# Optimization experiments

Measured on AMD Instinct MI355X. Metric: run time of the kernel, lower is better.

## Reference

```python
import jax, jax.numpy as jnp
import numpy as np

P = 2        # patch_size
HEADS = 1


def _conv(x, w, b, groups=1):
    # NCHW conv, kernel 3x3, SAME padding (stride 1)
    y = jax.lax.conv_general_dilated(
        x, w, window_strides=(1, 1), padding='SAME',
        dimension_numbers=('NCHW', 'OIHW', 'NCHW'),
        feature_group_count=groups)
    return y + b[None, :, None, None]


def _unfold(x, p):
    # torch.nn.Unfold(kernel=p, stride=p): [B,C,h,w] -> [B, C*p*p, n]
    B, C, h, w = x.shape
    x = x.reshape(B, C, h // p, p, w // p, p)
    x = x.transpose(0, 1, 3, 5, 2, 4)  # (B, C, ph, pw, h/p, w/p)
    return x.reshape(B, C * p * p, (h // p) * (w // p))


def _fold(x, p, h, w):
    # inverse of _unfold (non-overlapping patches)
    B = x.shape[0]
    C = x.shape[1] // (p * p)
    x = x.reshape(B, C, p, p, h // p, w // p)
    x = x.transpose(0, 1, 4, 2, 5, 3)  # (B, C, h/p, ph, w/p, pw)
    return x.reshape(B, C, h, w)


def setup_inputs() -> dict:
    key = jax.random.key(0)
    ks = jax.random.split(key, 9)
    c = 64
    x = jax.random.normal(ks[0], (2, 5, c, 64, 64), jnp.float32)
    wq = jax.random.normal(ks[1], (c, 1, 3, 3), jnp.float32) * 0.1
    bq = jax.random.normal(ks[2], (c,), jnp.float32) * 0.1
    wk = jax.random.normal(ks[3], (c, 1, 3, 3), jnp.float32) * 0.1
    bk = jax.random.normal(ks[4], (c,), jnp.float32) * 0.1
    wv = jax.random.normal(ks[5], (c, c, 3, 3), jnp.float32) * 0.05
    bv = jax.random.normal(ks[6], (c,), jnp.float32) * 0.1
    wc = jax.random.normal(ks[7], (c, c, 3, 3), jnp.float32) * 0.05
    bc = jax.random.normal(ks[8], (c,), jnp.float32) * 0.1
    return {"x": x, "wq": wq, "bq": bq, "wk": wk, "bk": bk,
            "wv": wv, "bv": bv, "wc": wc, "bc": bc}


def reference(x, wq, bq, wk, bk, wv, bv, wc, bc):
    b, t, c, h, w = x.shape
    p, H = P, HEADS
    D = p * p * c           # 256
    d = D // H              # per-head dim
    n = (h // p) * (w // p)  # tokens per frame

    xf = x.reshape(b * t, c, h, w)
    q = _conv(xf, wq, bq, groups=c)   # depthwise
    k = _conv(xf, wk, bk, groups=c)   # depthwise
    v = _conv(xf, wv, bv)             # dense conv

    def to_tokens(y):
        # [bt, D, n] -> [b, H, d, t*n]
        u = _unfold(y, p).reshape(b, t, H, d, n)
        return u.transpose(0, 2, 3, 1, 4).reshape(b, H, d, t * n)

    uq, uk, uv = to_tokens(q), to_tokens(k), to_tokens(v)

    attn = jnp.einsum('bhdi,bhdj->bhij', uq, uk) * (d ** -0.5)
    attn = jax.nn.softmax(attn, axis=-1)           # [b,H,tn,tn]
    ax = jnp.einsum('bhij,bhdj->bhid', attn, uv)   # [b,H,tn,d]

    ax = ax.reshape(b, H, t, n, d).transpose(0, 2, 1, 4, 3).reshape(b * t, D, n)
    feat = _fold(ax, p, h, w)                      # [bt, c, h, w]
    out = _conv(feat, wc, bc).reshape(x.shape) + x
    return out
```

## Files before the change

### kernel.cpp

```cpp
#include <hip/hip_runtime.h>
#include <hip/hip_bf16.h>

typedef __attribute__((ext_vector_type(8))) short short8;
typedef __attribute__((ext_vector_type(8))) unsigned short ushort8;
typedef __attribute__((ext_vector_type(4))) unsigned short ushort4v;
typedef __attribute__((ext_vector_type(4))) float f32x4;

#define NTOK 5120
#define DDIM 256
#define NJC 8

__device__ __forceinline__ unsigned short f2bf(float f) {
  union { float f; unsigned int u; } x; x.f = f;
  unsigned int r = x.u + 0x7FFFu + ((x.u >> 16) & 1u);
  return (unsigned short)(r >> 16);
}
__device__ __forceinline__ float bf2f(unsigned short u) {
  union { unsigned int i; float f; } x; x.i = ((unsigned int)u) << 16; return x.f;
}

__global__ __launch_bounds__(256) void qk_gen(
    const float* __restrict__ xin, const float* __restrict__ wq,
    const float* __restrict__ bq, const float* __restrict__ wk,
    const float* __restrict__ bk, unsigned short* __restrict__ qt,
    unsigned short* __restrict__ kt)
{
  const int ch = blockIdx.x;
  const int bt = blockIdx.y;
  const int b = bt / 5, tf = bt % 5;
  const int tid = threadIdx.x;
  const float* xp = xin + ((size_t)bt * 64 + ch) * 4096;
  float wqv[9], wkv[9];
  #pragma unroll
  for (int i = 0; i < 9; i++) { wqv[i] = wq[ch * 9 + i]; wkv[i] = wk[ch * 9 + i]; }
  const float bqv = bq[ch], bkv = bk[ch];

  #pragma unroll
  for (int p = 0; p < 4; p++) {
    int pid = tid + p * 256;
    int gy = pid >> 5, gx = pid & 31;
    float v[4][4];
    #pragma unroll
    for (int r = 0; r < 4; r++) {
      int yy = 2 * gy - 1 + r;
      #pragma unroll
      for (int cc = 0; cc < 4; cc++) {
        int xx = 2 * gx - 1 + cc;
        bool ok = (yy >= 0) && (yy < 64) && (xx >= 0) && (xx < 64);
        v[r][cc] = ok ? xp[yy * 64 + xx] : 0.f;
      }
    }
    unsigned short qo[4], ko[4];
    #pragma unroll
    for (int py = 0; py < 2; py++)
      #pragma unroll
      for (int px = 0; px < 2; px++) {
        float aq = bqv, ak = bkv;
        #pragma unroll
        for (int dy = 0; dy < 3; dy++)
          #pragma unroll
          for (int dx = 0; dx < 3; dx++) {
            float xv = v[py + dy][px + dx];
            aq += wqv[dy * 3 + dx] * xv;
            ak += wkv[dy * 3 + dx] * xv;
          }
        qo[py * 2 + px] = f2bf(aq);
        ko[py * 2 + px] = f2bf(ak);
      }
    size_t base = ((size_t)(b * NTOK + tf * 1024 + pid)) * DDIM + ch * 4;
    ushort4v qv = { qo[0], qo[1], qo[2], qo[3] };
    ushort4v kv = { ko[0], ko[1], ko[2], ko[3] };
    *(ushort4v*)(qt + base) = qv;
    *(ushort4v*)(kt + base) = kv;
  }
}

__global__ __launch_bounds__(256) void wt_gen(
    const float* __restrict__ w0, const float* __restrict__ w1,
    unsigned short* __restrict__ o0, unsigned short* __restrict__ o1)
{
  const int tap = blockIdx.x;
  const float* src = blockIdx.y ? w1 : w0;
  unsigned short* dst = blockIdx.y ? o1 : o0;
  const int t = threadIdx.x;
  #pragma unroll
  for (int i = 0; i < 16; i++) {
    int oi = t + i * 256;
    dst[tap * 4096 + oi] = f2bf(src[(size_t)oi * 9 + tap]);
  }
}

template<int MODE>
__global__ __launch_bounds__(256) void conv_mfma(
    const float* __restrict__ src, const unsigned short* __restrict__ wt,
    const float* __restrict__ bias, const float* __restrict__ resid,
    float* __restrict__ dstf, unsigned short* __restrict__ vt)
{
  const int strip = blockIdx.x;
  const int bt = blockIdx.y;
  const int y0 = strip * 2;
  const int tid = threadIdx.x;
  const int sw = tid >> 6, lane = tid & 63;
  const int ry = sw >> 1, ch = sw & 1;
  const int g = lane >> 4, c = lane & 15;

  __shared__ __align__(16) unsigned short lds_in[4 * 66 * 64];
  __shared__ __align__(16) unsigned short lds_w[64 * 64];

  {
    const int rr = lane >> 4;
    const int cb = lane & 15;
    const int row = y0 - 1 + rr;
    const bool rok = (row >= 0) && (row < 64);
    #pragma unroll
    for (int pp = 0; pp < 8; ++pp) {
      const int ci0 = sw * 16 + pp * 2;
      f32x4 va = { 0.f, 0.f, 0.f, 0.f }, vb = { 0.f, 0.f, 0.f, 0.f };
      if (rok) {
        va = *(const f32x4*)(src + ((size_t)(bt * 64 + ci0)) * 4096 + row * 64 + cb * 4);
        vb = *(const f32x4*)(src + ((size_t)(bt * 64 + ci0 + 1)) * 4096 + row * 64 + cb * 4);
      }
      char* rbase = (char*)lds_in + (rr * 66) * 128 + (ci0 & 7) * 2;
      const int sl = ci0 >> 3;
      #pragma unroll
      for (int q = 0; q < 4; ++q) {
        int lcol = cb * 4 + q + 1;
        unsigned int pk = (unsigned int)f2bf(va[q]) | ((unsigned int)f2bf(vb[q]) << 16);
        *(unsigned int*)(rbase + lcol * 128 + ((sl ^ (lcol & 7)) * 16)) = pk;
      }
      if (cb == 0)  *(unsigned int*)(rbase + ((sl ^ 0) * 16)) = 0u;
      if (cb == 15) *(unsigned int*)(rbase + 65 * 128 + ((sl ^ 1) * 16)) = 0u;
    }
  }

  f32x4 acc[2][4];
  #pragma unroll
  for (int ct = 0; ct < 2; ct++)
    #pragma unroll
    for (int xt = 0; xt < 4; xt++) acc[ct][xt] = (f32x4){ 0.f, 0.f, 0.f, 0.f };

  #pragma unroll 1
  for (int tap = 0; tap < 9; ++tap) {
    __syncthreads();
    {
      const unsigned short* wp = wt + tap * 4096;
      #pragma unroll
      for (int h = 0; h < 2; ++h) {
        int el = h * 2048 + tid * 8;
        int co = el >> 6, sl = (el & 63) >> 3;
        short8 wv8 = *(const short8*)(wp + el);
        *(short8*)((char*)lds_w + co * 128 + ((sl ^ (co & 7)) * 16)) = wv8;
      }
    }
    __syncthreads();
    const int dy = tap / 3 - 1, dx = tap % 3 - 1;
    const int rowp = ry + 1 + dy;
    #pragma unroll
    for (int kblk = 0; kblk < 2; ++kblk) {
      short8 af[2], bf[4];
      #pragma unroll
      for (int ct = 0; ct < 2; ++ct) {
        int co = ch * 32 + ct * 16 + c;
        af[ct] = *(const short8*)((char*)lds_w + co * 128 + (((kblk * 4 + g) ^ (co & 7)) * 16));
      }
      #pragma unroll
      for (int xt = 0; xt < 4; ++xt) {
        int lcol = xt * 16 + c + dx + 1;
        bf[xt] = *(const short8*)((char*)lds_in + (rowp * 66 + lcol) * 128 + (((kblk * 4 + g) ^ (lcol & 7)) * 16));
      }
      #pragma unroll
      for (int ct = 0; ct < 2; ++ct)
        #pragma unroll
        for (int xt = 0; xt < 4; ++xt)
          acc[ct][xt] = __builtin_amdgcn_mfma_f32_16x16x32_bf16(af[ct], bf[xt], acc[ct][xt], 0, 0, 0);
    }
  }

  const int y = y0 + ry;
  if (MODE == 0) {
    const int b = bt / 5, tf = bt % 5;
    const int py = y & 1, gy = y >> 1;
    #pragma unroll
    for (int ct = 0; ct < 2; ++ct)
      #pragma unroll
      for (int r = 0; r < 4; ++r) {
        const int co = ch * 32 + ct * 16 + g * 4 + r;
        const float bv = bias[co];
        #pragma unroll
        for (int xt = 0; xt < 4; ++xt) {
          int x = xt * 16 + c;
          int d = co * 4 + py * 2 + (x & 1);
          int tok = tf * 1024 + gy * 32 + (x >> 1);
          vt[((size_t)(b * DDIM + d)) * NTOK + tok] = f2bf(acc[ct][xt][r] + bv);
        }
      }
  } else {
    #pragma unroll
    for (int ct = 0; ct < 2; ++ct)
      #pragma unroll
      for (int r = 0; r < 4; ++r) {
        const int co = ch * 32 + ct * 16 + g * 4 + r;
        const float bv = bias[co];
        const size_t rowb = ((size_t)(bt * 64 + co)) * 4096 + (size_t)y * 64;
        #pragma unroll
        for (int xt = 0; xt < 4; ++xt) {
          int x = xt * 16 + c;
          dstf[rowb + x] = acc[ct][xt][r] + bv + resid[rowb + x];
        }
      }
  }
}

__global__ __launch_bounds__(256) void attn_kernel(
    const unsigned short* __restrict__ qt, const unsigned short* __restrict__ kt,
    const unsigned short* __restrict__ vt, float* __restrict__ po,
    float* __restrict__ pm, float* __restrict__ pl)
{
  const int wgid = blockIdx.x;
  const int chunk = wgid / 320;
  const int within = wgid % 320;
  const int slice = chunk * 8 + (within & 7);
  const int b = slice >> 3;
  const int jc = slice & 7;
  const int i0 = (within >> 3) * 128;
  const int jchunk = NTOK / NJC;
  const int tid = threadIdx.x;
  const int w = tid >> 6, lane = tid & 63;
  const int g = lane >> 4, c = lane & 15;

  __shared__ __align__(16) unsigned short lds_k[64 * 256];
  __shared__ __align__(16) unsigned short lds_v[256 * 64];
  __shared__ __align__(16) unsigned short lds_p[4 * 16 * 64];

  short8 qf[2][8];
  #pragma unroll
  for (int st = 0; st < 2; st++) {
    const unsigned short* qr = qt + ((size_t)(b * NTOK + i0 + w * 32 + st * 16 + c)) * DDIM + g * 8;
    #pragma unroll
    for (int kb = 0; kb < 8; kb++) qf[st][kb] = *(const short8*)(qr + kb * 32);
  }
  f32x4 o[32];
  #pragma unroll
  for (int i = 0; i < 32; i++) o[i] = (f32x4){ 0.f, 0.f, 0.f, 0.f };
  float m[2][4], l[2][4];
  #pragma unroll
  for (int st = 0; st < 2; st++)
    #pragma unroll
    for (int r = 0; r < 4; r++) { m[st][r] = -1e30f; l[st][r] = 0.f; }

  const int sr = tid >> 5, sc = tid & 31;
  const int vdr = tid >> 3, vcc = tid & 7;
  char* pb = (char*)lds_p + w * 2048;

  const int jbeg = jc * jchunk;
  for (int j0 = jbeg; j0 < jbeg + jchunk; j0 += 64) {
    #pragma unroll
    for (int p = 0; p < 8; p++) {
      int row = sr + p * 8;
      short8 kv = *(const short8*)(kt + ((size_t)(b * NTOK + j0 + row)) * DDIM + sc * 8);
      *(short8*)((char*)lds_k + row * 512 + ((sc ^ (row & 7)) * 16)) = kv;
    }
    #pragma unroll
    for (int p = 0; p < 8; p++) {
      int dd = vdr + p * 32;
      short8 vv = *(const short8*)(vt + ((size_t)(b * DDIM + dd)) * NTOK + j0 + vcc * 8);
      *(short8*)((char*)lds_v + dd * 128 + ((vcc ^ (dd & 7)) * 16)) = vv;
    }
    __syncthreads();

    f32x4 s0[4], s1[4];
    #pragma unroll
    for (int js = 0; js < 4; js++) {
      s0[js] = (f32x4){ 0.f, 0.f, 0.f, 0.f };
      s1[js] = (f32x4){ 0.f, 0.f, 0.f, 0.f };
      int row = js * 16 + c;
      int sw2 = row & 7;
      #pragma unroll
      for (int kb = 0; kb < 8; kb++) {
        short8 kf = *(const short8*)((char*)lds_k + row * 512 + (((kb * 4 + g) ^ sw2) * 16));
        s0[js] = __builtin_amdgcn_mfma_f32_16x16x32_bf16(qf[0][kb], kf, s0[js], 0, 0, 0);
        s1[js] = __builtin_amdgcn_mfma_f32_16x16x32_bf16(qf[1][kb], kf, s1[js], 0, 0, 0);
      }
    }
    short8 pf[2][2];
    {
      float pvv[4][4], alpha[4];
      #pragma unroll
      for (int r = 0; r < 4; r++) {
        float mx = fmaxf(fmaxf(s0[0][r], s0[1][r]), fmaxf(s0[2][r], s0[3][r])) * 0.0625f;
        #pragma unroll
        for (int off = 1; off < 16; off <<= 1) mx = fmaxf(mx, __shfl_xor(mx, off));
        float mn = fmaxf(m[0][r], mx);
        alpha[r] = __expf(m[0][r] - mn);
        float p0 = __expf(s0[0][r] * 0.0625f - mn);
        float p1 = __expf(s0[1][r] * 0.0625f - mn);
        float p2 = __expf(s0[2][r] * 0.0625f - mn);
        float p3 = __expf(s0[3][r] * 0.0625f - mn);
        pvv[0][r] = p0; pvv[1][r] = p1; pvv[2][r] = p2; pvv[3][r] = p3;
        float sum = p0 + p1 + p2 + p3;
        #pragma unroll
        for (int off = 1; off < 16; off <<= 1) sum += __shfl_xor(sum, off);
        l[0][r] = l[0][r] * alpha[r] + sum;
        m[0][r] = mn;
      }
      f32x4 av = { alpha[0], alpha[1], alpha[2], alpha[3] };
      #pragma unroll
      for (int ds = 0; ds < 16; ds++) o[ds] *= av;
      #pragma unroll
      for (int js = 0; js < 4; js++)
        #pragma unroll
        for (int r = 0; r < 4; r++) {
          int row = 4 * g + r;
          int slot = (js * 2 + (c >> 3)) ^ (row & 7);
          *(unsigned short*)(pb + row * 128 + slot * 16 + (c & 7) * 2) = f2bf(pvv[js][r]);
        }
      #pragma unroll
      for (int k2 = 0; k2 < 2; k2++)
        pf[0][k2] = *(short8*)(pb + c * 128 + (((k2 * 4 + g) ^ (c & 7)) * 16));
    }
    {
      float pvv[4][4], alpha[4];
      #pragma unroll
      for (int r = 0; r < 4; r++) {
        float mx = fmaxf(fmaxf(s1[0][r], s1[1][r]), fmaxf(s1[2][r], s1[3][r])) * 0.0625f;
        #pragma unroll
        for (int off = 1; off < 16; off <<= 1) mx = fmaxf(mx, __shfl_xor(mx, off));
        float mn = fmaxf(m[1][r], mx);
        alpha[r] = __expf(m[1][r] - mn);
        float p0 = __expf(s1[0][r] * 0.0625f - mn);
        float p1 = __expf(s1[1][r] * 0.0625f - mn);
        float p2 = __expf(s1[2][r] * 0.0625f - mn);
        float p3 = __expf(s1[3][r] * 0.0625f - mn);
        pvv[0][r] = p0; pvv[1][r] = p1; pvv[2][r] = p2; pvv[3][r] = p3;
        float sum = p0 + p1 + p2 + p3;
        #pragma unroll
        for (int off = 1; off < 16; off <<= 1) sum += __shfl_xor(sum, off);
        l[1][r] = l[1][r] * alpha[r] + sum;
        m[1][r] = mn;
      }
      f32x4 av = { alpha[0], alpha[1], alpha[2], alpha[3] };
      #pragma unroll
      for (int ds = 0; ds < 16; ds++) o[16 + ds] *= av;
      #pragma unroll
      for (int js = 0; js < 4; js++)
        #pragma unroll
        for (int r = 0; r < 4; r++) {
          int row = 4 * g + r;
          int slot = (js * 2 + (c >> 3)) ^ (row & 7);
          *(unsigned short*)(pb + row * 128 + slot * 16 + (c & 7) * 2) = f2bf(pvv[js][r]);
        }
      #pragma unroll
      for (int k2 = 0; k2 < 2; k2++)
        pf[1][k2] = *(short8*)(pb + c * 128 + (((k2 * 4 + g) ^ (c & 7)) * 16));
    }
    #pragma unroll
    for (int ds = 0; ds < 16; ds++) {
      int vrow = ds * 16 + c;
      int sw2 = c & 7;
      #pragma unroll
      for (int k2 = 0; k2 < 2; k2++) {
        short8 vf = *(const short8*)((char*)lds_v + vrow * 128 + (((k2 * 4 + g) ^ sw2) * 16));
        o[ds]      = __builtin_amdgcn_mfma_f32_16x16x32_bf16(pf[0][k2], vf, o[ds], 0, 0, 0);
        o[16 + ds] = __builtin_amdgcn_mfma_f32_16x16x32_bf16(pf[1][k2], vf, o[16 + ds], 0, 0, 0);
      }
    }
    __syncthreads();
  }
  #pragma unroll
  for (int st = 0; st < 2; st++) {
    const size_t rbase = ((size_t)(b * NJC + jc)) * NTOK + i0 + w * 32 + st * 16;
    #pragma unroll
    for (int ds = 0; ds < 16; ds++)
      #pragma unroll
      for (int r = 0; r < 4; r++)
        po[(rbase + 4 * g + r) * DDIM + ds * 16 + c] = o[st * 16 + ds][r];
    if (c == 0) {
      #pragma unroll
      for (int r = 0; r < 4; r++) {
        pm[rbase + 4 * g + r] = m[st][r];
        pl[rbase + 4 * g + r] = l[st][r];
      }
    }
  }
}

__global__ __launch_bounds__(256) void attn_combine(
    const float* __restrict__ po, const float* __restrict__ pm,
    const float* __restrict__ pl, float* __restrict__ feat, int njc)
{
  const int b = blockIdx.y;
  const int i0 = blockIdx.x * 64;
  const int t = threadIdx.x;
  const int row = t >> 2, dq = (t & 3) * 64;
  const int i = i0 + row;

  float M = -1e30f, L = 0.f;
  f32x4 acc[16];
  #pragma unroll
  for (int q = 0; q < 16; q++) acc[q] = (f32x4){ 0.f, 0.f, 0.f, 0.f };

  #pragma unroll 1
  for (int jc = 0; jc < njc; jc++) {
    const size_t rb = ((size_t)(b * njc + jc)) * NTOK + i;
    float mj = pm[rb], lj = pl[rb];
    float mn = fmaxf(M, mj);
    float so = __expf(M - mn), sn = __expf(mj - mn);
    const float* pp = po + rb * DDIM + dq;
    #pragma unroll
    for (int q = 0; q < 16; q++) {
      f32x4 v = *(const f32x4*)(pp + q * 4);
      acc[q] = acc[q] * so + v * sn;
    }
    L = L * so + lj * sn;
    M = mn;
  }
  const float inv = 1.f / L;
  const int tf = i >> 10, jn = i & 1023;
  const int gy = jn >> 5, gx = jn & 31;
  const size_t fb = ((size_t)((b * 5 + tf) * 64)) * 4096 + (2 * gy) * 64 + 2 * gx;
  #pragma unroll
  for (int q = 0; q < 16; q++) {
    f32x4 a = acc[q] * inv;
    int ch = (dq + q * 4) >> 2;
    size_t base = fb + (size_t)ch * 4096;
    feat[base] = a[0]; feat[base + 1] = a[1];
    feat[base + 64] = a[2]; feat[base + 65] = a[3];
  }
}

extern "C" void kernel_launch(void* const* d_in, const int* in_sizes, int n_in,
                              void* d_out, int out_size, void* d_ws, size_t ws_size,
                              hipStream_t stream) {
  const float* x  = (const float*)d_in[0];
  const float* wq = (const float*)d_in[1];
  const float* bq = (const float*)d_in[2];
  const float* wk = (const float*)d_in[3];
  const float* bk = (const float*)d_in[4];
  const float* wv = (const float*)d_in[5];
  const float* bv = (const float*)d_in[6];
  const float* wc = (const float*)d_in[7];
  const float* bc = (const float*)d_in[8];
  float* out = (float*)d_out;

  char* ws = (char*)d_ws;
  unsigned short* qt = (unsigned short*)(ws);
  unsigned short* kt = (unsigned short*)(ws + 5242880);
  unsigned short* vt = (unsigned short*)(ws + 10485760);
  float*          ft = (float*)(ws + 15728640);
  unsigned short* wtv = (unsigned short*)(ws + 26214400);
  unsigned short* wtc = (unsigned short*)(ws + 26288128);
  const size_t big_off = 26361856;
  float* po = (float*)(ws + big_off);

  size_t po_bytes = (size_t)2 * NJC * NTOK * DDIM * 4;
  float* pm = (float*)(ws + big_off + po_bytes);
  float* pl = pm + (size_t)2 * NJC * NTOK;

  wt_gen        <<<dim3(9, 2), 256, 0, stream>>>(wv, wc, wtv, wtc);
  qk_gen        <<<dim3(64, 10), 256, 0, stream>>>(x, wq, bq, wk, bk, qt, kt);
  conv_mfma<0>  <<<dim3(32, 10), 256, 0, stream>>>(x, wtv, bv, nullptr, nullptr, vt);
  attn_kernel   <<<dim3(640), 256, 0, stream>>>(qt, kt, vt, po, pm, pl);
  attn_combine  <<<dim3(80, 2), 256, 0, stream>>>(po, pm, pl, ft, NJC);
  conv_mfma<1>  <<<dim3(32, 10), 256, 0, stream>>>(ft, wtc, bc, x, out, nullptr);
}
```

Before: 246.0 us.

## Register-prefetch next K/V tile and skip O rescale when max unchanged

Loads the next 64-key K and V tiles from global memory into registers right after the LDS barrier, so the global load latency overlaps the QK^T MFMAs and softmax of the current tile. Also skips the output accumulator rescale when no row maximum changed anywhere in the wavefront. The prefetch adds 16 short8 registers per thread on top of an already large accumulator set, which may raise register pressure and lower occupancy. The rescale skip adds a wave vote and a branch.

```diff
diff --git a/kernel.cpp b/kernel.cpp
--- a/kernel.cpp
+++ b/kernel.cpp
@@ -253,20 +253,37 @@
   char* pb = (char*)lds_p + w * 2048;
 
   const int jbeg = jc * jchunk;
-  for (int j0 = jbeg; j0 < jbeg + jchunk; j0 += 64) {
+  const int jend = jbeg + jchunk;
+
+  short8 kpre[8], vpre[8];
+  #pragma unroll
+  for (int p = 0; p < 8; p++) {
+    int row = sr + p * 8;
+    kpre[p] = *(const short8*)(kt + ((size_t)(b * NTOK + jbeg + row)) * DDIM + sc * 8);
+    int dd = vdr + p * 32;
+    vpre[p] = *(const short8*)(vt + ((size_t)(b * DDIM + dd)) * NTOK + jbeg + vcc * 8);
+  }
+
+  for (int j0 = jbeg; j0 < jend; j0 += 64) {
     #pragma unroll
     for (int p = 0; p < 8; p++) {
       int row = sr + p * 8;
-      short8 kv = *(const short8*)(kt + ((size_t)(b * NTOK + j0 + row)) * DDIM + sc * 8);
-      *(short8*)((char*)lds_k + row * 512 + ((sc ^ (row & 7)) * 16)) = kv;
-    }
-    #pragma unroll
-    for (int p = 0; p < 8; p++) {
+      *(short8*)((char*)lds_k + row * 512 + ((sc ^ (row & 7)) * 16)) = kpre[p];
       int dd = vdr + p * 32;
-      short8 vv = *(const short8*)(vt + ((size_t)(b * DDIM + dd)) * NTOK + j0 + vcc * 8);
-      *(short8*)((char*)lds_v + dd * 128 + ((vcc ^ (dd & 7)) * 16)) = vv;
+      *(short8*)((char*)lds_v + dd * 128 + ((vcc ^ (dd & 7)) * 16)) = vpre[p];
     }
     __syncthreads();
+
+    if (j0 + 64 < jend) {
+      const int jn = j0 + 64;
+      #pragma unroll
+      for (int p = 0; p < 8; p++) {
+        int row = sr + p * 8;
+        kpre[p] = *(const short8*)(kt + ((size_t)(b * NTOK + jn + row)) * DDIM + sc * 8);
+        int dd = vdr + p * 32;
+        vpre[p] = *(const short8*)(vt + ((size_t)(b * DDIM + dd)) * NTOK + jn + vcc * 8);
+      }
+    }
 
     f32x4 s0[4], s1[4];
     #pragma unroll
@@ -285,13 +302,16 @@
     short8 pf[2][2];
     {
       float pvv[4][4], alpha[4];
+      int need = 0;
       #pragma unroll
       for (int r = 0; r < 4; r++) {
         float mx = fmaxf(fmaxf(s0[0][r], s0[1][r]), fmaxf(s0[2][r], s0[3][r])) * 0.0625f;
         #pragma unroll
         for (int off = 1; off < 16; off <<= 1) mx = fmaxf(mx, __shfl_xor(mx, off));
-        float mn = fmaxf(m[0][r], mx);
-        alpha[r] = __expf(m[0][r] - mn);
+        float mold = m[0][r];
+        float mn = fmaxf(mold, mx);
+        alpha[r] = __expf(mold - mn);
+        if (mn > mold) need = 1;
         float p0 = __expf(s0[0][r] * 0.0625f - mn);
         float p1 = __expf(s0[1][r] * 0.0625f - mn);
         float p2 = __expf(s0[2][r] * 0.0625f - mn);
@@ -303,9 +323,11 @@
         l[0][r] = l[0][r] * alpha[r] + sum;
         m[0][r] = mn;
       }
-      f32x4 av = { alpha[0], alpha[1], alpha[2], alpha[3] };
-      #pragma unroll
-      for (int ds = 0; ds < 16; ds++) o[ds] *= av;
+      if (__any(need)) {
+        f32x4 av = { alpha[0], alpha[1], alpha[2], alpha[3] };
+        #pragma unroll
+        for (int ds = 0; ds < 16; ds++) o[ds] *= av;
+      }
       #pragma unroll
       for (int js = 0; js < 4; js++)
         #pragma unroll
@@ -320,13 +342,16 @@
     }
     {
       float pvv[4][4], alpha[4];
+      int need = 0;
       #pragma unroll
       for (int r = 0; r < 4; r++) {
         float mx = fmaxf(fmaxf(s1[0][r], s1[1][r]), fmaxf(s1[2][r], s1[3][r])) * 0.0625f;
         #pragma unroll
         for (int off = 1; off < 16; off <<= 1) mx = fmaxf(mx, __shfl_xor(mx, off));
-        float mn = fmaxf(m[1][r], mx);
-        alpha[r] = __expf(m[1][r] - mn);
+        float mold = m[1][r];
+        float mn = fmaxf(mold, mx);
+        alpha[r] = __expf(mold - mn);
+        if (mn > mold) need = 1;
         float p0 = __expf(s1[0][r] * 0.0625f - mn);
         float p1 = __expf(s1[1][r] * 0.0625f - mn);
         float p2 = __expf(s1[2][r] * 0.0625f - mn);
@@ -338,9 +363,11 @@
         l[1][r] = l[1][r] * alpha[r] + sum;
         m[1][r] = mn;
       }
-      f32x4 av = { alpha[0], alpha[1], alpha[2], alpha[3] };
-      #pragma unroll
-      for (int ds = 0; ds < 16; ds++) o[16 + ds] *= av;
+      if (__any(need)) {
+        f32x4 av = { alpha[0], alpha[1], alpha[2], alpha[3] };
+        #pragma unroll
+        for (int ds = 0; ds < 16; ds++) o[16 + ds] *= av;
+      }
       #pragma unroll
       for (int js = 0; js < 4; js++)
         #pragma unroll
```

New measurement: 283.3 us. 15.1% more time.

## Halve attention query tile per wave and switch softmax to exp2 domain

Applied to the files above, without the earlier changes.

Each wave now handles 16 query rows instead of 32, so each workgroup covers 64 rows and twice as many workgroups (1280) are launched. The accumulator shrinks from 32 to 16 f32x4 registers, which should raise occupancy and improve latency hiding. The cost is that K/V tiles are loaded into LDS twice as often per query row, doubling global/LDS traffic for K and V. The softmax scale is also folded with log2(e) so exp2f replaces __expf, and the combine kernel uses exp2f to match.

```diff
diff --git a/kernel.cpp b/kernel.cpp
--- a/kernel.cpp
+++ b/kernel.cpp
@@ -217,12 +217,12 @@
     float* __restrict__ pm, float* __restrict__ pl)
 {
   const int wgid = blockIdx.x;
-  const int chunk = wgid / 320;
-  const int within = wgid % 320;
+  const int chunk = wgid / 640;
+  const int within = wgid % 640;
   const int slice = chunk * 8 + (within & 7);
   const int b = slice >> 3;
   const int jc = slice & 7;
-  const int i0 = (within >> 3) * 128;
+  const int i0 = (within >> 3) * 64;
   const int jchunk = NTOK / NJC;
   const int tid = threadIdx.x;
   const int w = tid >> 6, lane = tid & 63;
@@ -232,21 +232,19 @@
   __shared__ __align__(16) unsigned short lds_v[256 * 64];
   __shared__ __align__(16) unsigned short lds_p[4 * 16 * 64];
 
-  short8 qf[2][8];
-  #pragma unroll
-  for (int st = 0; st < 2; st++) {
-    const unsigned short* qr = qt + ((size_t)(b * NTOK + i0 + w * 32 + st * 16 + c)) * DDIM + g * 8;
-    #pragma unroll
-    for (int kb = 0; kb < 8; kb++) qf[st][kb] = *(const short8*)(qr + kb * 32);
-  }
-  f32x4 o[32];
-  #pragma unroll
-  for (int i = 0; i < 32; i++) o[i] = (f32x4){ 0.f, 0.f, 0.f, 0.f };
-  float m[2][4], l[2][4];
-  #pragma unroll
-  for (int st = 0; st < 2; st++)
-    #pragma unroll
-    for (int r = 0; r < 4; r++) { m[st][r] = -1e30f; l[st][r] = 0.f; }
+  const float C2 = 0.0625f * 1.4426950408889634f;
+
+  short8 qf[8];
+  {
+    const unsigned short* qr = qt + ((size_t)(b * NTOK + i0 + w * 16 + c)) * DDIM + g * 8;
+    #pragma unroll
+    for (int kb = 0; kb < 8; kb++) qf[kb] = *(const short8*)(qr + kb * 32);
+  }
+  f32x4 o[16];
+  #pragma unroll
+  for (int i = 0; i < 16; i++) o[i] = (f32x4){ 0.f, 0.f, 0.f, 0.f };
+  float m[4] = { -1e30f, -1e30f, -1e30f, -1e30f };
+  float l[4] = { 0.f, 0.f, 0.f, 0.f };
 
   const int sr = tid >> 5, sc = tid & 31;
   const int vdr = tid >> 3, vcc = tid & 7;
@@ -268,91 +266,55 @@
     }
     __syncthreads();
 
-    f32x4 s0[4], s1[4];
+    f32x4 s[4];
     #pragma unroll
     for (int js = 0; js < 4; js++) {
-      s0[js] = (f32x4){ 0.f, 0.f, 0.f, 0.f };
-      s1[js] = (f32x4){ 0.f, 0.f, 0.f, 0.f };
+      s[js] = (f32x4){ 0.f, 0.f, 0.f, 0.f };
       int row = js * 16 + c;
       int sw2 = row & 7;
       #pragma unroll
       for (int kb = 0; kb < 8; kb++) {
         short8 kf = *(const short8*)((char*)lds_k + row * 512 + (((kb * 4 + g) ^ sw2) * 16));
-        s0[js] = __builtin_amdgcn_mfma_f32_16x16x32_bf16(qf[0][kb], kf, s0[js], 0, 0, 0);
-        s1[js] = __builtin_amdgcn_mfma_f32_16x16x32_bf16(qf[1][kb], kf, s1[js], 0, 0, 0);
-      }
-    }
-    short8 pf[2][2];
+        s[js] = __builtin_amdgcn_mfma_f32_16x16x32_bf16(qf[kb], kf, s[js], 0, 0, 0);
+      }
+    }
+    float pvv[4][4], alpha[4];
+    #pragma unroll
+    for (int r = 0; r < 4; r++) {
+      float t0 = s[0][r] * C2, t1 = s[1][r] * C2, t2 = s[2][r] * C2, t3 = s[3][r] * C2;
+      float mx = fmaxf(fmaxf(t0, t1), fmaxf(t2, t3));
+      #pragma unroll
+      for (int off = 1; off < 16; off <<= 1) mx = fmaxf(mx, __shfl_xor(mx, off));
+      float mn = fmaxf(m[r], mx);
+      alpha[r] = exp2f(m[r] - mn);
+      float p0 = exp2f(t0 - mn);
+      float p1 = exp2f(t1 - mn);
+      float p2 = exp2f(t2 - mn);
+      float p3 = exp2f(t3 - mn);
+      pvv[0][r] = p0; pvv[1][r] = p1; pvv[2][r] = p2; pvv[3][r] = p3;
+      float sum = p0 + p1 + p2 + p3;
+      #pragma unroll
+      for (int off = 1; off < 16; off <<= 1) sum += __shfl_xor(sum, off);
+      l[r] = l[r] * alpha[r] + sum;
+      m[r] = mn;
+    }
     {
-      float pvv[4][4], alpha[4];
+      f32x4 av = { alpha[0], alpha[1], alpha[2], alpha[3] };
+      #pragma unroll
+      for (int ds = 0; ds < 16; ds++) o[ds] *= av;
+    }
+    #pragma unroll
+    for (int js = 0; js < 4; js++)
       #pragma unroll
       for (int r = 0; r < 4; r++) {
-        float mx = fmaxf(fmaxf(s0[0][r], s0[1][r]), fmaxf(s0[2][r], s0[3][r])) * 0.0625f;
-        #pragma unroll
-        for (int off = 1; off < 16; off <<= 1) mx = fmaxf(mx, __shfl_xor(mx, off));
-        float mn = fmaxf(m[0][r], mx);
-        alpha[r] = __expf(m[0][r] - mn);
-        float p0 = __expf(s0[0][r] * 0.0625f - mn);
-        float p1 = __expf(s0[1][r] * 0.0625f - mn);
-        float p2 = __expf(s0[2][r] * 0.0625f - mn);
-        float p3 = __expf(s0[3][r] * 0.0625f - mn);
-        pvv[0][r] = p0; pvv[1][r] = p1; pvv[2][r] = p2; pvv[3][r] = p3;
-        float sum = p0 + p1 + p2 + p3;
-        #pragma unroll
-        for (int off = 1; off < 16; off <<= 1) sum += __shfl_xor(sum, off);
-        l[0][r] = l[0][r] * alpha[r] + sum;
-        m[0][r] = mn;
-      }
-      f32x4 av = { alpha[0], alpha[1], alpha[2], alpha[3] };
-      #pragma unroll
-      for (int ds = 0; ds < 16; ds++) o[ds] *= av;
-      #pragma unroll
-      for (int js = 0; js < 4; js++)
-        #pragma unroll
-        for (int r = 0; r < 4; r++) {
-          int row = 4 * g + r;
-          int slot = (js * 2 + (c >> 3)) ^ (row & 7);
-          *(unsigned short*)(pb + row * 128 + slot * 16 + (c & 7) * 2) = f2bf(pvv[js][r]);
-        }
-      #pragma unroll
-      for (int k2 = 0; k2 < 2; k2++)
-        pf[0][k2] = *(short8*)(pb + c * 128 + (((k2 * 4 + g) ^ (c & 7)) * 16));
-    }
-    {
-      float pvv[4][4], alpha[4];
-      #pragma unroll
-      for (int r = 0; r < 4; r++) {
-        float mx = fmaxf(fmaxf(s1[0][r], s1[1][r]), fmaxf(s1[2][r], s1[3][r])) * 0.0625f;
-        #pragma unroll
-        for (int off = 1; off < 16; off <<= 1) mx = fmaxf(mx, __shfl_xor(mx, off));
-        float mn = fmaxf(m[1][r], mx);
-        alpha[r] = __expf(m[1][r] - mn);
-        float p0 = __expf(s1[0][r] * 0.0625f - mn);
-        float p1 = __expf(s1[1][r] * 0.0625f - mn);
-        float p2 = __expf(s1[2][r] * 0.0625f - mn);
-        float p3 = __expf(s1[3][r] * 0.0625f - mn);
-        pvv[0][r] = p0; pvv[1][r] = p1; pvv[2][r] = p2; pvv[3][r] = p3;
-        float sum = p0 + p1 + p2 + p3;
-        #pragma unroll
-        for (int off = 1; off < 16; off <<= 1) sum += __shfl_xor(sum, off);
-        l[1][r] = l[1][r] * alpha[r] + sum;
-        m[1][r] = mn;
-      }
-      f32x4 av = { alpha[0], alpha[1], alpha[2], alpha[3] };
-      #pragma unroll
-      for (int ds = 0; ds < 16; ds++) o[16 + ds] *= av;
-      #pragma unroll
-      for (int js = 0; js < 4; js++)
-        #pragma unroll
-        for (int r = 0; r < 4; r++) {
-          int row = 4 * g + r;
-          int slot = (js * 2 + (c >> 3)) ^ (row & 7);
-          *(unsigned short*)(pb + row * 128 + slot * 16 + (c & 7) * 2) = f2bf(pvv[js][r]);
-        }
-      #pragma unroll
-      for (int k2 = 0; k2 < 2; k2++)
-        pf[1][k2] = *(short8*)(pb + c * 128 + (((k2 * 4 + g) ^ (c & 7)) * 16));
-    }
+        int row = 4 * g + r;
+        int slot = (js * 2 + (c >> 3)) ^ (row & 7);
+        *(unsigned short*)(pb + row * 128 + slot * 16 + (c & 7) * 2) = f2bf(pvv[js][r]);
+      }
+    short8 pf[2];
+    #pragma unroll
+    for (int k2 = 0; k2 < 2; k2++)
+      pf[k2] = *(short8*)(pb + c * 128 + (((k2 * 4 + g) ^ (c & 7)) * 16));
     #pragma unroll
     for (int ds = 0; ds < 16; ds++) {
       int vrow = ds * 16 + c;
@@ -360,25 +322,23 @@
       #pragma unroll
       for (int k2 = 0; k2 < 2; k2++) {
         short8 vf = *(const short8*)((char*)lds_v + vrow * 128 + (((k2 * 4 + g) ^ sw2) * 16));
-        o[ds]      = __builtin_amdgcn_mfma_f32_16x16x32_bf16(pf[0][k2], vf, o[ds], 0, 0, 0);
-        o[16 + ds] = __builtin_amdgcn_mfma_f32_16x16x32_bf16(pf[1][k2], vf, o[16 + ds], 0, 0, 0);
+        o[ds] = __builtin_amdgcn_mfma_f32_16x16x32_bf16(pf[k2], vf, o[ds], 0, 0, 0);
       }
     }
     __syncthreads();
   }
-  #pragma unroll
-  for (int st = 0; st < 2; st++) {
-    const size_t rbase = ((size_t)(b * NJC + jc)) * NTOK + i0 + w * 32 + st * 16;
+  {
+    const size_t rbase = ((size_t)(b * NJC + jc)) * NTOK + i0 + w * 16;
     #pragma unroll
     for (int ds = 0; ds < 16; ds++)
       #pragma unroll
       for (int r = 0; r < 4; r++)
-        po[(rbase + 4 * g + r) * DDIM + ds * 16 + c] = o[st * 16 + ds][r];
+        po[(rbase + 4 * g + r) * DDIM + ds * 16 + c] = o[ds][r];
     if (c == 0) {
       #pragma unroll
       for (int r = 0; r < 4; r++) {
-        pm[rbase + 4 * g + r] = m[st][r];
-        pl[rbase + 4 * g + r] = l[st][r];
+        pm[rbase + 4 * g + r] = m[r];
+        pl[rbase + 4 * g + r] = l[r];
       }
     }
   }
@@ -404,7 +364,7 @@
     const size_t rb = ((size_t)(b * njc + jc)) * NTOK + i;
     float mj = pm[rb], lj = pl[rb];
     float mn = fmaxf(M, mj);
-    float so = __expf(M - mn), sn = __expf(mj - mn);
+    float so = exp2f(M - mn), sn = exp2f(mj - mn);
     const float* pp = po + rb * DDIM + dq;
     #pragma unroll
     for (int q = 0; q < 16; q++) {
@@ -459,7 +419,7 @@
   wt_gen        <<<dim3(9, 2), 256, 0, stream>>>(wv, wc, wtv, wtc);
   qk_gen        <<<dim3(64, 10), 256, 0, stream>>>(x, wq, bq, wk, bk, qt, kt);
   conv_mfma<0>  <<<dim3(32, 10), 256, 0, stream>>>(x, wtv, bv, nullptr, nullptr, vt);
-  attn_kernel   <<<dim3(640), 256, 0, stream>>>(qt, kt, vt, po, pm, pl);
+  attn_kernel   <<<dim3(1280), 256, 0, stream>>>(qt, kt, vt, po, pm, pl);
   attn_combine  <<<dim3(80, 2), 256, 0, stream>>>(po, pm, pl, ft, NJC);
   conv_mfma<1>  <<<dim3(32, 10), 256, 0, stream>>>(ft, wtc, bc, x, out, nullptr);
 }
```

Result: slower. 442.6 us (+79.9%).
